# Performance work log

Measured on AMD Instinct MI355X. Metric: run time of the kernel, lower is better.

## Reference

```python
import jax, jax.numpy as jnp
import numpy as np

B, T, C, H = 4, 4096, 1024, 16
HD = C // H  # 64


def setup_inputs() -> dict:
    key = jax.random.key(0)
    k1, k2, k3, k4 = jax.random.split(key, 4)
    x = jax.random.normal(k1, (B, T, C), dtype=jnp.float32)
    Wqkv = jax.random.normal(k2, (3 * C, C), dtype=jnp.float32) * (1.0 / np.sqrt(C))
    Wout = jax.random.normal(k3, (C, C), dtype=jnp.float32) * (1.0 / np.sqrt(C))
    bout = jax.random.normal(k4, (C,), dtype=jnp.float32) * 0.02
    return {"x": x, "Wqkv": Wqkv, "Wout": Wout, "bout": bout}


def reference(x, Wqkv, Wout, bout):
    # qkv projection (torch Linear: y = x @ W.T)
    qkv = x @ Wqkv.T                              # (B, T, 3C)
    qkv = qkv.reshape(B, T, H, 3 * HD)            # view(B, T, heads, 3*head_dim)
    q, k, v = jnp.split(qkv, 3, axis=-1)          # each (B, T, H, HD)
    # NOTE: faithful to source: q @ k.transpose(-2,-1) batches over (B,T)
    # and contracts head_dim -> attention over the HEADS axis, shape (B,T,H,H).
    att = jnp.einsum("bthd,btgd->bthg", q, k) / np.float32(np.sqrt(HD))
    att = jax.nn.softmax(att, axis=-1)            # softmax over heads axis g
    out = jnp.einsum("bthg,btgd->bthd", att, v)   # (B, T, H, HD)
    out = out.reshape(B, T, C)
    return out @ Wout.T + bout
```

## Files before the change

kernel.cpp:

```cpp
#include <hip/hip_runtime.h>
#include <hip/hip_bf16.h>
#include <stdint.h>

typedef __attribute__((ext_vector_type(8))) short bf16x8;
typedef __attribute__((ext_vector_type(4))) float f32x4;
typedef unsigned short ushort_t;

__device__ __forceinline__ float b2f(unsigned short u) {
  union { unsigned u32; float f; } c; c.u32 = ((unsigned)u) << 16; return c.f;
}
__device__ __forceinline__ unsigned short f2b(float f) {
  union { float f; unsigned u; } c; c.f = f;
  unsigned u = c.u;
  return (unsigned short)((u + 0x7FFFu + ((u >> 16) & 1u)) >> 16);
}

__global__ __launch_bounds__(256) void cast_f32_bf16(const float* __restrict__ in,
                                                     unsigned short* __restrict__ out,
                                                     int n8) {
  int i = blockIdx.x * 256 + threadIdx.x;
  if (i >= n8) return;
  const float4* p = (const float4*)in + (size_t)i * 2;
  float4 a = p[0], b = p[1];
  union { bf16x8 v; unsigned short s[8]; } o;
  o.s[0] = f2b(a.x); o.s[1] = f2b(a.y); o.s[2] = f2b(a.z); o.s[3] = f2b(a.w);
  o.s[4] = f2b(b.x); o.s[5] = f2b(b.y); o.s[6] = f2b(b.z); o.s[7] = f2b(b.w);
  ((bf16x8*)out)[i] = o.v;
}

#define GLDS16(g, l)                                                          \
  __builtin_amdgcn_global_load_lds((const __attribute__((address_space(1))) void*)(g), \
                                   (__attribute__((address_space(3))) void*)(l), 16, 0, 0)

#define BAR1()                                             \
  __builtin_amdgcn_s_barrier();                            \
  asm volatile("s_waitcnt lgkmcnt(0)" ::: "memory");       \
  __builtin_amdgcn_sched_barrier(0)

#define BAR2()                                             \
  __builtin_amdgcn_sched_barrier(0);                       \
  __builtin_amdgcn_s_barrier();                            \
  asm volatile("" ::: "memory")

#define VM4() asm volatile("s_waitcnt vmcnt(4)" ::: "memory")

template <typename OutT, bool BIAS>
__global__ __launch_bounds__(512, 2) void gemm8p(const unsigned short* __restrict__ A,
                                                 const unsigned short* __restrict__ B,
                                                 OutT* __restrict__ C,
                                                 const float* __restrict__ bias,
                                                 int M, int N, int K) {
  __shared__ ushort_t smA[2 * 16384];
  __shared__ ushort_t smB[2 * 16384];

  const int tid  = threadIdx.x;
  const int lane = tid & 63;
  const int wave = tid >> 6;
  const int wm = wave >> 2;
  const int wn = wave & 3;
  const int tileM = blockIdx.y * 256;
  const int tileN = blockIdx.x * 256;
  const int NT = K >> 6;

  const int srow = tid >> 3;
  const int sg   = (tid & 7) ^ (srow & 7);
  const unsigned short* Abase = A + (size_t)(tileM + srow) * K + sg * 8;
  const unsigned short* Bbase = B + (size_t)(tileN + srow) * K + sg * 8;

#define STAGE_A(h, tt, pp) {                                                   \
    const unsigned short* s_ = Abase + (size_t)(h) * 128 * K + (size_t)(tt) * 64; \
    GLDS16(s_, &smA[(pp) * 16384 + (h) * 8192 + tid * 8]);                     \
    GLDS16(s_ + (size_t)64 * K, &smA[(pp) * 16384 + (h) * 8192 + 4096 + tid * 8]); }
#define STAGE_B(h, tt, pp) {                                                   \
    const unsigned short* s_ = Bbase + (size_t)(h) * 128 * K + (size_t)(tt) * 64; \
    GLDS16(s_, &smB[(pp) * 16384 + (h) * 8192 + tid * 8]);                     \
    GLDS16(s_ + (size_t)64 * K, &smB[(pp) * 16384 + (h) * 8192 + 4096 + tid * 8]); }

  const int lr  = lane & 15;
  const int kg  = lane >> 4;
  const int gx0 = kg ^ (lr & 7);
  const int gx1 = gx0 ^ 4;
#define LDSA(pp, row, gx) (*(const bf16x8*)&smA[(pp) * 16384 + (row) * 64 + ((gx) << 3)])
#define LDSB(pp, row, gx) (*(const bf16x8*)&smB[(pp) * 16384 + (row) * 64 + ((gx) << 3)])

  f32x4 acc[8][4] = {};
  bf16x8 af[4], bf[4];

#define MFMA16(mh)                                                   \
  __builtin_amdgcn_s_setprio(1);                                     \
  _Pragma("unroll") for (int m = 0; m < 4; ++m)                      \
    _Pragma("unroll") for (int n = 0; n < 4; ++n)                    \
      acc[(mh) * 4 + m][n] =                                         \
          __builtin_amdgcn_mfma_f32_16x16x32_bf16(af[m], bf[n], acc[(mh) * 4 + m][n], 0, 0, 0); \
  __builtin_amdgcn_s_setprio(0)

  STAGE_A(0, 0, 0); STAGE_A(1, 0, 0); STAGE_B(0, 0, 0); STAGE_B(1, 0, 0);
  STAGE_A(0, 1, 1);
  asm volatile("s_waitcnt vmcnt(2)" ::: "memory");
  __builtin_amdgcn_s_barrier();
  asm volatile("" ::: "memory");

  const int arow0 = wm * 64 + lr;
  const int brow0 = wn * 64 + lr;

  for (int t = 0; t < NT; ++t) {
    const int p  = t & 1;
    const int pn = p ^ 1;
    const bool s1 = (t + 1) < NT;
    const bool s2 = (t + 2) < NT;

#pragma unroll
    for (int n = 0; n < 4; ++n) bf[n] = LDSB(p, brow0 + n * 16, gx0);
#pragma unroll
    for (int m = 0; m < 4; ++m) af[m] = LDSA(p, arow0 + m * 16, gx0);
    if (s1) STAGE_B(0, t + 1, pn);
    BAR1();
    MFMA16(0);
    VM4();
    BAR2();

#pragma unroll
    for (int m = 0; m < 4; ++m) af[m] = LDSA(p, 128 + arow0 + m * 16, gx0);
    if (s1) STAGE_B(1, t + 1, pn);
    BAR1();
    MFMA16(1);
    BAR2();

#pragma unroll
    for (int n = 0; n < 4; ++n) bf[n] = LDSB(p, brow0 + n * 16, gx1);
#pragma unroll
    for (int m = 0; m < 4; ++m) af[m] = LDSA(p, arow0 + m * 16, gx1);
    if (s1) STAGE_A(1, t + 1, pn);
    BAR1();
    MFMA16(0);
    BAR2();

#pragma unroll
    for (int m = 0; m < 4; ++m) af[m] = LDSA(p, 128 + arow0 + m * 16, gx1);
    if (s2) STAGE_A(0, t + 2, p);
    BAR1();
    MFMA16(1);
    VM4();
    BAR2();
  }

  const int crow0 = (lane >> 4) * 4;
  const int ccol  = lane & 15;
#pragma unroll
  for (int n = 0; n < 4; ++n) {
    const int col = tileN + wn * 64 + n * 16 + ccol;
    float bv = 0.f;
    if (BIAS) bv = bias[col];
#pragma unroll
    for (int m = 0; m < 8; ++m) {
      const int row = tileM + (m >> 2) * 128 + wm * 64 + (m & 3) * 16 + crow0;
#pragma unroll
      for (int j = 0; j < 4; ++j) {
        float v = acc[m][n][j] + bv;
        if constexpr (sizeof(OutT) == 2)
          ((unsigned short*)C)[(size_t)(row + j) * N + col] = f2b(v);
        else
          ((float*)C)[(size_t)(row + j) * N + col] = v;
      }
    }
  }
}

__global__ __launch_bounds__(256) void attn_heads(const unsigned short* __restrict__ qkv,
                                                  unsigned short* __restrict__ attout) {
  __shared__ float kvs[4][2][16 * 64];
  const int wave = threadIdx.x >> 6;
  const int lane = threadIdx.x & 63;
  const size_t tok = (size_t)blockIdx.x * 4 + wave;
  const int h = lane >> 2;
  const int s = lane & 3;

  const unsigned short* base = qkv + tok * 3072 + h * 192 + s * 16;
  bf16x8 q0 = *(const bf16x8*)(base);
  bf16x8 q1 = *(const bf16x8*)(base + 8);
  bf16x8 k0 = *(const bf16x8*)(base + 64);
  bf16x8 k1 = *(const bf16x8*)(base + 72);
  bf16x8 v0 = *(const bf16x8*)(base + 128);
  bf16x8 v1 = *(const bf16x8*)(base + 136);

  float q[16], kr[16], vr[16];
#pragma unroll
  for (int j = 0; j < 8; ++j) {
    q[j]      = b2f((unsigned short)q0[j]);
    q[8 + j]  = b2f((unsigned short)q1[j]);
    kr[j]     = b2f((unsigned short)k0[j]);
    kr[8 + j] = b2f((unsigned short)k1[j]);
    vr[j]     = b2f((unsigned short)v0[j]);
    vr[8 + j] = b2f((unsigned short)v1[j]);
  }

  float* kb = kvs[wave][0];
  float* vb = kvs[wave][1];
#pragma unroll
  for (int c = 0; c < 4; ++c) {
    const int off = h * 64 + (((s * 4 + c) * 4) ^ ((h & 7) << 2));
    *(float4*)&kb[off] = make_float4(kr[c * 4], kr[c * 4 + 1], kr[c * 4 + 2], kr[c * 4 + 3]);
    *(float4*)&vb[off] = make_float4(vr[c * 4], vr[c * 4 + 1], vr[c * 4 + 2], vr[c * 4 + 3]);
  }

  float att[16];
#pragma unroll
  for (int g = 0; g < 16; ++g) {
    float a = 0.f;
#pragma unroll
    for (int c = 0; c < 4; ++c) {
      const int off = g * 64 + (((s * 4 + c) * 4) ^ ((g & 7) << 2));
      float4 kf = *(const float4*)&kb[off];
      a += q[c * 4 + 0] * kf.x + q[c * 4 + 1] * kf.y +
           q[c * 4 + 2] * kf.z + q[c * 4 + 3] * kf.w;
    }
    a += __shfl_xor(a, 1);
    a += __shfl_xor(a, 2);
    att[g] = a * 0.125f;
  }

  float mx = att[0];
#pragma unroll
  for (int g = 1; g < 16; ++g) mx = fmaxf(mx, att[g]);
  float sum = 0.f;
#pragma unroll
  for (int g = 0; g < 16; ++g) { att[g] = __expf(att[g] - mx); sum += att[g]; }
  const float inv = 1.f / sum;

  float o[16];
#pragma unroll
  for (int j = 0; j < 16; ++j) o[j] = 0.f;
#pragma unroll
  for (int g = 0; g < 16; ++g) {
    const float pg = att[g];
#pragma unroll
    for (int c = 0; c < 4; ++c) {
      const int off = g * 64 + (((s * 4 + c) * 4) ^ ((g & 7) << 2));
      float4 vf = *(const float4*)&vb[off];
      o[c * 4 + 0] += pg * vf.x;
      o[c * 4 + 1] += pg * vf.y;
      o[c * 4 + 2] += pg * vf.z;
      o[c * 4 + 3] += pg * vf.w;
    }
  }

  union { bf16x8 v[2]; unsigned short u[16]; } ob;
#pragma unroll
  for (int j = 0; j < 16; ++j) ob.u[j] = f2b(o[j] * inv);
  bf16x8* dst = (bf16x8*)&attout[tok * 1024 + h * 64 + s * 16];
  dst[0] = ob.v[0];
  dst[1] = ob.v[1];
}

extern "C" void kernel_launch(void* const* d_in, const int* in_sizes, int n_in,
                              void* d_out, int out_size, void* d_ws, size_t ws_size,
                              hipStream_t stream) {
  const float* x    = (const float*)d_in[0];
  const float* Wqkv = (const float*)d_in[1];
  const float* Wout = (const float*)d_in[2];
  const float* bout = (const float*)d_in[3];
  float* out = (float*)d_out;

  char* ws = (char*)d_ws;
  unsigned short* xb     = (unsigned short*)(ws);
  unsigned short* wqkvb  = (unsigned short*)(ws + 33554432);
  unsigned short* woutb  = (unsigned short*)(ws + 39845888);
  unsigned short* qkv    = (unsigned short*)(ws + 41943040);
  unsigned short* attout = (unsigned short*)(ws + 142606336);

  cast_f32_bf16<<<8192, 256, 0, stream>>>(x, xb, 2097152);
  cast_f32_bf16<<<1536, 256, 0, stream>>>(Wqkv, wqkvb, 393216);
  cast_f32_bf16<<<512, 256, 0, stream>>>(Wout, woutb, 131072);

  gemm8p<unsigned short, false><<<dim3(12, 64), 512, 0, stream>>>(
      xb, wqkvb, qkv, nullptr, 16384, 3072, 1024);

  attn_heads<<<4096, 256, 0, stream>>>(qkv, attout);

  gemm8p<float, true><<<dim3(4, 64), 512, 0, stream>>>(
      attout, woutb, out, bout, 16384, 1024, 1024);
}
```

Measured before the change: 346.2 us.

## Use MFMA for per-token head attention and swizzle GEMM block order

The per-token 16x16 head attention moves from scalar FMA over LDS-staged fp32 K/V to two matrix-core instructions, one for QK^T and one for PV. Softmax now runs on the accumulator fragments using cross-lane shuffles. The GEMM also remaps block indices so consecutive workgroups spread across XCD-like groups, and its epilogue loop is reordered so columns vary fastest. The probabilities are rounded to bf16 before PV, a small loss of precision, and V is gathered and the output written with scalar 2-byte accesses.

```diff
diff --git a/kernel.cpp b/kernel.cpp
--- a/kernel.cpp
+++ b/kernel.cpp
@@ -3,6 +3,7 @@
 #include <stdint.h>
 
 typedef __attribute__((ext_vector_type(8))) short bf16x8;
+typedef __attribute__((ext_vector_type(4))) short bf16x4;
 typedef __attribute__((ext_vector_type(4))) float f32x4;
 typedef unsigned short ushort_t;
 
@@ -58,8 +59,12 @@
   const int wave = tid >> 6;
   const int wm = wave >> 2;
   const int wn = wave & 3;
-  const int tileM = blockIdx.y * 256;
-  const int tileN = blockIdx.x * 256;
+
+  const int nwg = gridDim.x * gridDim.y;
+  const int bid = blockIdx.y * gridDim.x + blockIdx.x;
+  const int swz = (bid & 7) * (nwg >> 3) + (bid >> 3);
+  const int tileM = (swz / gridDim.x) * 256;
+  const int tileN = (swz % gridDim.x) * 256;
   const int NT = K >> 6;
 
   const int srow = tid >> 3;
@@ -146,110 +151,95 @@
 
   const int crow0 = (lane >> 4) * 4;
   const int ccol  = lane & 15;
-#pragma unroll
-  for (int n = 0; n < 4; ++n) {
-    const int col = tileN + wn * 64 + n * 16 + ccol;
-    float bv = 0.f;
-    if (BIAS) bv = bias[col];
-#pragma unroll
-    for (int m = 0; m < 8; ++m) {
-      const int row = tileM + (m >> 2) * 128 + wm * 64 + (m & 3) * 16 + crow0;
-#pragma unroll
-      for (int j = 0; j < 4; ++j) {
-        float v = acc[m][n][j] + bv;
+  float bv[4];
+#pragma unroll
+  for (int n = 0; n < 4; ++n)
+    bv[n] = BIAS ? bias[tileN + wn * 64 + n * 16 + ccol] : 0.f;
+#pragma unroll
+  for (int m = 0; m < 8; ++m) {
+#pragma unroll
+    for (int j = 0; j < 4; ++j) {
+      const int row = tileM + (m >> 2) * 128 + wm * 64 + (m & 3) * 16 + crow0 + j;
+#pragma unroll
+      for (int n = 0; n < 4; ++n) {
+        const int col = tileN + wn * 64 + n * 16 + ccol;
+        float v = acc[m][n][j] + bv[n];
         if constexpr (sizeof(OutT) == 2)
-          ((unsigned short*)C)[(size_t)(row + j) * N + col] = f2b(v);
+          ((unsigned short*)C)[(size_t)row * N + col] = f2b(v);
         else
-          ((float*)C)[(size_t)(row + j) * N + col] = v;
+          ((float*)C)[(size_t)row * N + col] = v;
       }
     }
   }
 }
 
-__global__ __launch_bounds__(256) void attn_heads(const unsigned short* __restrict__ qkv,
-                                                  unsigned short* __restrict__ attout) {
-  __shared__ float kvs[4][2][16 * 64];
+static __device__ __forceinline__ f32x4 mfma_pv(bf16x4 a, bf16x4 b, f32x4 c) {
+#if __has_builtin(__builtin_amdgcn_mfma_f32_16x16x16_bf16)
+  return __builtin_amdgcn_mfma_f32_16x16x16_bf16(a, b, c, 0, 0, 0);
+#elif __has_builtin(__builtin_amdgcn_mfma_f32_16x16x16bf16_1k)
+  return __builtin_amdgcn_mfma_f32_16x16x16bf16_1k(a, b, c, 0, 0, 0);
+#else
+  f32x4 d;
+  asm volatile("v_mfma_f32_16x16x16_bf16 %0, %1, %2, %3"
+               : "=&v"(d) : "v"(a), "v"(b), "v"(c));
+  return d;
+#endif
+}
+
+__global__ __launch_bounds__(256) void attn_mfma(const unsigned short* __restrict__ qkv,
+                                                 unsigned short* __restrict__ attout) {
   const int wave = threadIdx.x >> 6;
   const int lane = threadIdx.x & 63;
+  const int lo = lane & 15;
+  const int hi = lane >> 4;
   const size_t tok = (size_t)blockIdx.x * 4 + wave;
-  const int h = lane >> 2;
-  const int s = lane & 3;
-
-  const unsigned short* base = qkv + tok * 3072 + h * 192 + s * 16;
-  bf16x8 q0 = *(const bf16x8*)(base);
-  bf16x8 q1 = *(const bf16x8*)(base + 8);
-  bf16x8 k0 = *(const bf16x8*)(base + 64);
-  bf16x8 k1 = *(const bf16x8*)(base + 72);
-  bf16x8 v0 = *(const bf16x8*)(base + 128);
-  bf16x8 v1 = *(const bf16x8*)(base + 136);
-
-  float q[16], kr[16], vr[16];
-#pragma unroll
-  for (int j = 0; j < 8; ++j) {
-    q[j]      = b2f((unsigned short)q0[j]);
-    q[8 + j]  = b2f((unsigned short)q1[j]);
-    kr[j]     = b2f((unsigned short)k0[j]);
-    kr[8 + j] = b2f((unsigned short)k1[j]);
-    vr[j]     = b2f((unsigned short)v0[j]);
-    vr[8 + j] = b2f((unsigned short)v1[j]);
-  }
-
-  float* kb = kvs[wave][0];
-  float* vb = kvs[wave][1];
+  const unsigned short* base = qkv + tok * 3072;
+
+  const unsigned short* krow = base + lo * 192 + 64 + hi * 8;
+  const unsigned short* qrow = base + lo * 192 + hi * 8;
+  bf16x8 ka0 = *(const bf16x8*)(krow);
+  bf16x8 ka1 = *(const bf16x8*)(krow + 32);
+  bf16x8 qb0 = *(const bf16x8*)(qrow);
+  bf16x8 qb1 = *(const bf16x8*)(qrow + 32);
+
+  f32x4 att = {};
+  att = __builtin_amdgcn_mfma_f32_16x16x32_bf16(ka0, qb0, att, 0, 0, 0);
+  att = __builtin_amdgcn_mfma_f32_16x16x32_bf16(ka1, qb1, att, 0, 0, 0);
+
+  float s0 = att[0] * 0.125f, s1 = att[1] * 0.125f;
+  float s2 = att[2] * 0.125f, s3 = att[3] * 0.125f;
+  float mx = fmaxf(fmaxf(s0, s1), fmaxf(s2, s3));
+  mx = fmaxf(mx, __shfl_xor(mx, 16));
+  mx = fmaxf(mx, __shfl_xor(mx, 32));
+  float e0 = __expf(s0 - mx), e1 = __expf(s1 - mx);
+  float e2 = __expf(s2 - mx), e3 = __expf(s3 - mx);
+  float sum = e0 + e1 + e2 + e3;
+  sum += __shfl_xor(sum, 16);
+  sum += __shfl_xor(sum, 32);
+  const float inv = 1.f / sum;
+
+  union { bf16x4 v; unsigned short u[4]; } pa;
+  pa.u[0] = f2b(e0 * inv); pa.u[1] = f2b(e1 * inv);
+  pa.u[2] = f2b(e2 * inv); pa.u[3] = f2b(e3 * inv);
+
+  f32x4 o[4];
 #pragma unroll
   for (int c = 0; c < 4; ++c) {
-    const int off = h * 64 + (((s * 4 + c) * 4) ^ ((h & 7) << 2));
-    *(float4*)&kb[off] = make_float4(kr[c * 4], kr[c * 4 + 1], kr[c * 4 + 2], kr[c * 4 + 3]);
-    *(float4*)&vb[off] = make_float4(vr[c * 4], vr[c * 4 + 1], vr[c * 4 + 2], vr[c * 4 + 3]);
-  }
-
-  float att[16];
-#pragma unroll
-  for (int g = 0; g < 16; ++g) {
-    float a = 0.f;
-#pragma unroll
-    for (int c = 0; c < 4; ++c) {
-      const int off = g * 64 + (((s * 4 + c) * 4) ^ ((g & 7) << 2));
-      float4 kf = *(const float4*)&kb[off];
-      a += q[c * 4 + 0] * kf.x + q[c * 4 + 1] * kf.y +
-           q[c * 4 + 2] * kf.z + q[c * 4 + 3] * kf.w;
-    }
-    a += __shfl_xor(a, 1);
-    a += __shfl_xor(a, 2);
-    att[g] = a * 0.125f;
-  }
-
-  float mx = att[0];
-#pragma unroll
-  for (int g = 1; g < 16; ++g) mx = fmaxf(mx, att[g]);
-  float sum = 0.f;
-#pragma unroll
-  for (int g = 0; g < 16; ++g) { att[g] = __expf(att[g] - mx); sum += att[g]; }
-  const float inv = 1.f / sum;
-
-  float o[16];
-#pragma unroll
-  for (int j = 0; j < 16; ++j) o[j] = 0.f;
-#pragma unroll
-  for (int g = 0; g < 16; ++g) {
-    const float pg = att[g];
-#pragma unroll
-    for (int c = 0; c < 4; ++c) {
-      const int off = g * 64 + (((s * 4 + c) * 4) ^ ((g & 7) << 2));
-      float4 vf = *(const float4*)&vb[off];
-      o[c * 4 + 0] += pg * vf.x;
-      o[c * 4 + 1] += pg * vf.y;
-      o[c * 4 + 2] += pg * vf.z;
-      o[c * 4 + 3] += pg * vf.w;
-    }
-  }
-
-  union { bf16x8 v[2]; unsigned short u[16]; } ob;
-#pragma unroll
-  for (int j = 0; j < 16; ++j) ob.u[j] = f2b(o[j] * inv);
-  bf16x8* dst = (bf16x8*)&attout[tok * 1024 + h * 64 + s * 16];
-  dst[0] = ob.v[0];
-  dst[1] = ob.v[1];
+    union { bf16x4 v; unsigned short u[4]; } vb;
+#pragma unroll
+    for (int j = 0; j < 4; ++j)
+      vb.u[j] = base[(4 * hi + j) * 192 + 128 + c * 16 + lo];
+    f32x4 z = {};
+    o[c] = mfma_pv(pa.v, vb.v, z);
+  }
+
+  unsigned short* dst = attout + tok * 1024;
+#pragma unroll
+  for (int jj = 0; jj < 4; ++jj) {
+#pragma unroll
+    for (int c = 0; c < 4; ++c)
+      dst[(4 * hi + jj) * 64 + c * 16 + lo] = f2b(o[c][jj]);
+  }
 }
 
 extern "C" void kernel_launch(void* const* d_in, const int* in_sizes, int n_in,
@@ -275,7 +265,7 @@
   gemm8p<unsigned short, false><<<dim3(12, 64), 512, 0, stream>>>(
       xb, wqkvb, qkv, nullptr, 16384, 3072, 1024);
 
-  attn_heads<<<4096, 256, 0, stream>>>(qkv, attout);
+  attn_mfma<<<4096, 256, 0, stream>>>(qkv, attout);
 
   gemm8p<float, true><<<dim3(4, 64), 512, 0, stream>>>(
       attout, woutb, out, bout, 16384, 1024, 1024);
```

Result: faster. 295.9 us (-14.5%).
